# Kernel tuning notes

Measured on AMD Instinct MI355X. Metric: run time of the kernel, lower is better.

The kernel has to match this reference:

```python
import jax, jax.numpy as jnp
import numpy as np

B, C, H, W = 8, 512, 64, 64
G = 32  # GroupNorm groups
EPS = 1e-5


def setup_inputs() -> dict:
    key = jax.random.key(0)
    ks = jax.random.split(key, 5)
    x = jax.random.normal(ks[0], (B, C, H, W), dtype=jnp.float32)
    gn_w = jnp.ones((C,), jnp.float32)
    gn_b = jnp.zeros((C,), jnp.float32)
    # 1x1 convs == channel-mixing matmuls; kaiming-ish init scale
    qkv_w = jax.random.normal(ks[1], (3 * C, C), jnp.float32) / np.sqrt(C)
    qkv_b = jnp.zeros((3 * C,), jnp.float32)
    proj_w = jax.random.normal(ks[2], (C, C), jnp.float32) / np.sqrt(C)
    proj_b = jnp.zeros((C,), jnp.float32)
    return {"x": x, "gn_w": gn_w, "gn_b": gn_b, "qkv_w": qkv_w,
            "qkv_b": qkv_b, "proj_w": proj_w, "proj_b": proj_b}


def _group_norm(x, w, b):
    Bv, Cv, Hv, Wv = x.shape
    xr = x.reshape(Bv, G, Cv // G, Hv * Wv)
    mu = xr.mean(axis=(2, 3), keepdims=True)
    var = xr.var(axis=(2, 3), keepdims=True)
    xn = ((xr - mu) * jax.lax.rsqrt(var + EPS)).reshape(Bv, Cv, Hv, Wv)
    return xn * w[None, :, None, None] + b[None, :, None, None]


def reference(x, gn_w, gn_b, qkv_w, qkv_b, proj_w, proj_b):
    Bv, Cv, Hv, Wv = x.shape
    T = Hv * Wv
    h = _group_norm(x, gn_w, gn_b)
    # 1x1 conv -> [B, 3C, T]
    qkv = jnp.einsum('bchw,oc->bohw', h, qkv_w) + qkv_b[None, :, None, None]
    qkv = qkv.reshape(Bv, 3, Cv, T)
    q, k, v = qkv[:, 0], qkv[:, 1], qkv[:, 2]  # each [B, C, T]
    scale = Cv ** -0.25  # 1/sqrt(sqrt(C)), applied to q and k
    attn = jnp.einsum('bct,bcs->bts', q * scale, k * scale)  # [B, T, T]
    attn = jax.nn.softmax(attn, axis=-1)
    out = jnp.einsum('bts,bcs->bct', attn, v).reshape(Bv, Cv, Hv, Wv)
    out = jnp.einsum('bchw,oc->bohw', out, proj_w) + proj_b[None, :, None, None]
    return x + out
```

## Files before the change

### kernel.cpp

```cpp
#include <hip/hip_runtime.h>

typedef unsigned short u16;
typedef unsigned int   u32;
typedef unsigned long long u64;

typedef __attribute__((ext_vector_type(8)))  short short8;
typedef __attribute__((ext_vector_type(4)))  short short4v;
typedef __attribute__((ext_vector_type(4)))  float float4v;
typedef __attribute__((ext_vector_type(16))) float float16v;

#define NB 8
#define NC 512
#define NT 4096
#define NO 1536
#define SCALE_QK 0.04419417382415922f
#define LOG2E_   1.4426950408889634f

__device__ inline u16 f2b(float f){
  u32 u = __builtin_bit_cast(u32, f);
  u += 0x7fffu + ((u >> 16) & 1u);
  return (u16)(u >> 16);
}

typedef __attribute__((address_space(1))) const unsigned int as1c_uint;
typedef __attribute__((address_space(3))) unsigned int as3_uint;

__device__ inline void gload16(const void* g, void* l){
  __builtin_amdgcn_global_load_lds((as1c_uint*)g, (as3_uint*)l, 16, 0, 0);
}

__device__ inline short8 ld8pair(const u16* p){
  short4v a = *(const short4v*)(p);
  short4v b = *(const short4v*)(p + 4);
  return __builtin_shufflevector(a, b, 0,1,2,3,4,5,6,7);
}

__global__ void k_cvt(const float* __restrict__ src, u16* __restrict__ dst, int n){
  int i = blockIdx.x*256 + threadIdx.x;
  if (i < n) dst[i] = f2b(src[i]);
}

__global__ void k_stats(const float* __restrict__ x, float* __restrict__ stats){
  int bg = blockIdx.x;
  int tid = threadIdx.x;
  const float4* p = (const float4*)(x + (size_t)bg*65536);
  float s = 0.f, q = 0.f;
  for (int i=0;i<64;i++){
    float4 v = p[i*256 + tid];
    s += v.x+v.y+v.z+v.w;
    q += v.x*v.x + v.y*v.y + v.z*v.z + v.w*v.w;
  }
  __shared__ float ls[256], lq[256];
  ls[tid]=s; lq[tid]=q; __syncthreads();
  for (int off=128; off>0; off>>=1){
    if (tid < off){ ls[tid]+=ls[tid+off]; lq[tid]+=lq[tid+off]; }
    __syncthreads();
  }
  if (tid==0){
    float mean = ls[0]*(1.f/65536.f);
    float var  = lq[0]*(1.f/65536.f) - mean*mean;
    stats[bg*2]   = mean;
    stats[bg*2+1] = rsqrtf(var + 1e-5f);
  }
}

__global__ void k_gn_apply(const float* __restrict__ x, const float* __restrict__ stats,
                           const float* __restrict__ gw, const float* __restrict__ gb,
                           u16* __restrict__ h){
  __shared__ u16 lt[64*65];
  int b = blockIdx.z, c0 = blockIdx.y*64, t0 = blockIdx.x*64;
  int tid = threadIdx.x;
  for (int it=0; it<16; it++){
    int idx = it*256 + tid;
    int cl = idx>>6, tl = idx&63;
    int c = c0 + cl;
    float v = x[((size_t)b*NC + c)*NT + t0 + tl];
    float mean = stats[(b*32 + (c>>4))*2];
    float rstd = stats[(b*32 + (c>>4))*2 + 1];
    float y = (v - mean)*rstd*gw[c] + gb[c];
    lt[cl*65 + tl] = f2b(y);
  }
  __syncthreads();
  for (int it=0; it<16; it++){
    int idx = it*256 + tid;
    int tw = idx>>6, cw = idx&63;
    h[((size_t)b*NT + t0 + tw)*NC + c0 + cw] = lt[cw*65 + tw];
  }
}

__device__ inline void stage128(const u16* gbase, u16* lbuf, int w, int l){
  #pragma unroll
  for (int i=0;i<4;i++){
    int r0 = (w*4+i)*8;
    int lr = r0 + (l>>3);
    int gch = (l&7) ^ (lr&7);
    gload16(gbase + (size_t)lr*512 + gch*8, lbuf + r0*64);
  }
}

__device__ inline void tile_mac(const u16* sA, const u16* sB, float4v acc[4][4], int wm, int wn, int l){
  #pragma unroll
  for (int kk=0; kk<2; kk++){
    short8 af[4], bf[4];
    #pragma unroll
    for (int f=0; f<4; f++){
      int rowA = wm + f*16 + (l&15);
      int chA  = (kk*4 + (l>>4)) ^ (rowA&7);
      af[f] = *(const short8*)(sA + rowA*64 + chA*8);
      int rowB = wn + f*16 + (l&15);
      int chB  = (kk*4 + (l>>4)) ^ (rowB&7);
      bf[f] = *(const short8*)(sB + rowB*64 + chB*8);
    }
    #pragma unroll
    for (int fm=0; fm<4; fm++)
      #pragma unroll
      for (int fn=0; fn<4; fn++)
        acc[fm][fn] = __builtin_amdgcn_mfma_f32_16x16x32_bf16(af[fm], bf[fn], acc[fm][fn], 0,0,0);
  }
}

__global__ __launch_bounds__(256,2) void k_qkv_gemm(const u16* __restrict__ h, const u16* __restrict__ wq,
                                                    const float* __restrict__ qb, u16* __restrict__ qkv){
  __shared__ __align__(16) u16 lA[2][8192];
  __shared__ __align__(16) u16 lB[2][8192];
  int b = blockIdx.z, t0 = blockIdx.y*128, o0 = blockIdx.x*128;
  int tid = threadIdx.x, w = tid>>6, l = tid&63;
  int wm = (w&1)*64, wn = (w>>1)*64;
  float4v acc[4][4];
  #pragma unroll
  for (int i=0;i<4;i++)
    #pragma unroll
    for (int j=0;j<4;j++)
      #pragma unroll
      for (int e=0;e<4;e++) acc[i][j][e] = 0.f;
  const u16* Ab = h  + ((size_t)b*NT + t0)*NC;
  const u16* Bb = wq + (size_t)o0*NC;
  stage128(Ab, lA[0], w, l);
  stage128(Bb, lB[0], w, l);
  __syncthreads();
  for (int it=0; it<8; it++){
    int cur = it&1;
    if (it < 7){
      stage128(Ab + (it+1)*64, lA[cur^1], w, l);
      stage128(Bb + (it+1)*64, lB[cur^1], w, l);
    }
    tile_mac(lA[cur], lB[cur], acc, wm, wn, l);
    __syncthreads();
  }
  u16* ep = ((w < 2) ? (u16*)lA : (u16*)lB) + (w&1)*4352;
  #pragma unroll
  for (int fn=0; fn<4; fn++){
    float bs = qb[o0 + wn + fn*16 + (l&15)];
    #pragma unroll
    for (int fm=0; fm<4; fm++)
      #pragma unroll
      for (int r=0; r<4; r++){
        int tl_ = fm*16 + (l>>4)*4 + r;
        int ol_ = fn*16 + (l&15);
        ep[tl_*68 + ol_] = f2b(acc[fm][fn][r] + bs);
      }
  }
  __syncthreads();
  #pragma unroll
  for (int i=0;i<8;i++){
    int r  = i*8 + (l>>3);
    int c8 = (l&7)*8;
    short8 v8 = ld8pair(ep + r*68 + c8);
    *(short8*)(qkv + ((size_t)b*NT + t0 + wm + r)*NO + o0 + wn + c8) = v8;
  }
}

__global__ void k_vtrans(const u16* __restrict__ qkv, u16* __restrict__ vct){
  __shared__ u16 lt[64*65];
  int b = blockIdx.z, c0 = blockIdx.y*64, t0 = blockIdx.x*64;
  int tid = threadIdx.x;
  for (int it=0; it<16; it++){
    int idx = it*256 + tid;
    int tl = idx>>6, cl = idx&63;
    lt[tl*65 + cl] = qkv[((size_t)b*NT + t0+tl)*NO + 1024 + c0 + cl];
  }
  __syncthreads();
  for (int it=0; it<16; it++){
    int idx = it*256 + tid;
    int cw = idx>>6, tw = idx&63;
    vct[((size_t)b*NC + c0+cw)*NT + t0 + tw] = lt[tw*65 + cw];
  }
}

__global__ __launch_bounds__(256,2) void k_attn(const u16* __restrict__ qkv, const u16* __restrict__ vct,
                                                u16* __restrict__ at){
  __shared__ __align__(16) u16 lK[32*512];
  __shared__ __align__(16) u16 lV[512*36];
  __shared__ __align__(16) u16 lP[64*36];
  __shared__ __align__(16) float lAl[64];
  __shared__ __align__(16) float lLs[64];
  const int b = blockIdx.y, t0 = blockIdx.x*64;
  const int tid = threadIdx.x, w = tid>>6, l = tid&63;
  const int l15 = l&15, l4 = l>>4, l31 = l&31, l5 = l>>5;
  const int mq = w, pm = w>>1, pc = w&1;

  short8 qf[16];
  {
    const u16* qrow = qkv + ((size_t)b*NT + t0 + mq*16 + l15)*NO;
    #pragma unroll
    for (int ks=0; ks<16; ks++) qf[ks] = *(const short8*)(qrow + ks*32 + l4*8);
  }
  float16v acc[8];
  #pragma unroll
  for (int i=0;i<8;i++)
    #pragma unroll
    for (int j=0;j<16;j++) acc[i][j] = 0.f;
  float M_r[4] = {-1e30f,-1e30f,-1e30f,-1e30f};
  float L_r[4] = {0.f,0.f,0.f,0.f};

  for (int st=0; st<128; st++){
    const int s0 = st*32;
    #pragma unroll
    for (int i=0;i<8;i++){
      int sl = w*8 + i;
      const u16* krow = qkv + ((size_t)b*NT + s0 + sl)*NO + 512;
      gload16(krow + (l ^ (sl&7))*8, &lK[sl*512]);
    }
    #pragma unroll
    for (int rr=0; rr<2; rr++){
      int c = rr*256 + tid;
      const u64* vr = (const u64*)(vct + ((size_t)b*NC + c)*NT + s0);
      u64* dst = (u64*)(&lV[c*36]);
      #pragma unroll
      for (int i=0;i<8;i++) dst[i] = vr[i];
    }
    __syncthreads();

    float4v Lf0, Lf1;
    #pragma unroll
    for (int e=0;e<4;e++){ Lf0[e]=0.f; Lf1[e]=0.f; }
    #pragma unroll
    for (int ks=0; ks<16; ks++){
      int gch = ks*4 + l4;
      int sA = l15;
      short8 b0 = *(const short8*)(&lK[sA*512 + ((gch ^ (sA&7))*8)]);
      int sB = 16 + l15;
      short8 b1 = *(const short8*)(&lK[sB*512 + ((gch ^ (sB&7))*8)]);
      Lf0 = __builtin_amdgcn_mfma_f32_16x16x32_bf16(qf[ks], b0, Lf0, 0,0,0);
      Lf1 = __builtin_amdgcn_mfma_f32_16x16x32_bf16(qf[ks], b1, Lf1, 0,0,0);
    }
    #pragma unroll
    for (int r=0; r<4; r++){
      float v0 = Lf0[r]*SCALE_QK, v1 = Lf1[r]*SCALE_QK;
      float mx = fmaxf(v0, v1);
      mx = fmaxf(mx, __shfl_xor(mx,1));
      mx = fmaxf(mx, __shfl_xor(mx,2));
      mx = fmaxf(mx, __shfl_xor(mx,4));
      mx = fmaxf(mx, __shfl_xor(mx,8));
      float mnew = fmaxf(M_r[r], mx);
      float al = exp2f((M_r[r] - mnew)*LOG2E_);
      float p0 = exp2f((v0 - mnew)*LOG2E_);
      float p1 = exp2f((v1 - mnew)*LOG2E_);
      float sum = p0 + p1;
      sum += __shfl_xor(sum,1); sum += __shfl_xor(sum,2);
      sum += __shfl_xor(sum,4); sum += __shfl_xor(sum,8);
      L_r[r] = L_r[r]*al + sum;
      M_r[r] = mnew;
      int tl_ = mq*16 + l4*4 + r;
      lP[tl_*36 + l15]      = f2b(p0);
      lP[tl_*36 + 16 + l15] = f2b(p1);
      if (l15 == 0) lAl[tl_] = al;
    }
    __syncthreads();

    {
      float4v a_[4];
      #pragma unroll
      for (int q=0;q<4;q++) a_[q] = *(const float4v*)(&lAl[pm*32 + q*8 + l5*4]);
      #pragma unroll
      for (int fn=0; fn<8; fn++)
        #pragma unroll
        for (int q=0;q<4;q++)
          #pragma unroll
          for (int rr=0;rr<4;rr++) acc[fn][q*4+rr] *= a_[q][rr];

      const u16* prow = &lP[(pm*32 + l31)*36];
      short8 pa0 = ld8pair(prow + l5*8);
      short8 pa1 = ld8pair(prow + 16 + l5*8);
      #pragma unroll
      for (int fn=0; fn<8; fn++){
        const u16* vrow = &lV[(pc*256 + fn*32 + l31)*36];
        short8 vb0 = ld8pair(vrow + l5*8);
        short8 vb1 = ld8pair(vrow + 16 + l5*8);
        acc[fn] = __builtin_amdgcn_mfma_f32_32x32x16_bf16(pa0, vb0, acc[fn], 0,0,0);
        acc[fn] = __builtin_amdgcn_mfma_f32_32x32x16_bf16(pa1, vb1, acc[fn], 0,0,0);
      }
    }
    __syncthreads();
  }

  if (l15 == 0){
    #pragma unroll
    for (int r=0;r<4;r++) lLs[mq*16 + l4*4 + r] = L_r[r];
  }
  __syncthreads();
  {
    float4v iv[4];
    #pragma unroll
    for (int q=0;q<4;q++){
      float4v t_ = *(const float4v*)(&lLs[pm*32 + q*8 + l5*4]);
      #pragma unroll
      for (int rr=0;rr<4;rr++) iv[q][rr] = 1.f/t_[rr];
    }
    #pragma unroll
    for (int fn=0; fn<8; fn++){
      int cc = pc*256 + fn*32 + l31;
      #pragma unroll
      for (int q=0;q<4;q++)
        #pragma unroll
        for (int rr=0;rr<4;rr++){
          int tt = t0 + pm*32 + rr + q*8 + l5*4;
          at[((size_t)b*NT + tt)*NC + cc] = f2b(acc[fn][q*4+rr]*iv[q][rr]);
        }
    }
  }
}

__global__ __launch_bounds__(256,2) void k_proj_res(const u16* __restrict__ wp, const u16* __restrict__ at,
                                                    const float* __restrict__ pb, const float* __restrict__ x,
                                                    float* __restrict__ out){
  __shared__ __align__(16) u16 lA[2][8192];
  __shared__ __align__(16) u16 lB[2][8192];
  int b = blockIdx.z, t0 = blockIdx.x*128, o0 = blockIdx.y*128;
  int tid = threadIdx.x, w = tid>>6, l = tid&63;
  int wm = (w&1)*64, wn = (w>>1)*64;
  float4v acc[4][4];
  #pragma unroll
  for (int i=0;i<4;i++)
    #pragma unroll
    for (int j=0;j<4;j++)
      #pragma unroll
      for (int e=0;e<4;e++) acc[i][j][e] = 0.f;
  const u16* Ab = wp + (size_t)o0*NC;
  const u16* Bb = at + ((size_t)b*NT + t0)*NC;
  stage128(Ab, lA[0], w, l);
  stage128(Bb, lB[0], w, l);
  __syncthreads();
  for (int it=0; it<8; it++){
    int cur = it&1;
    if (it < 7){
      stage128(Ab + (it+1)*64, lA[cur^1], w, l);
      stage128(Bb + (it+1)*64, lB[cur^1], w, l);
    }
    tile_mac(lA[cur], lB[cur], acc, wm, wn, l);
    __syncthreads();
  }
  #pragma unroll
  for (int fm=0; fm<4; fm++)
    #pragma unroll
    for (int r=0; r<4; r++){
      int o = o0 + wm + fm*16 + (l>>4)*4 + r;
      float bs = pb[o];
      #pragma unroll
      for (int fn=0; fn<4; fn++){
        int t = t0 + wn + fn*16 + (l&15);
        size_t idx = ((size_t)b*NC + o)*NT + t;
        out[idx] = acc[fm][fn][r] + bs + x[idx];
      }
    }
}

extern "C" void kernel_launch(void* const* d_in, const int* in_sizes, int n_in,
                              void* d_out, int out_size, void* d_ws, size_t ws_size,
                              hipStream_t stream){
  const float* x    = (const float*)d_in[0];
  const float* gnw  = (const float*)d_in[1];
  const float* gnb  = (const float*)d_in[2];
  const float* qkvw = (const float*)d_in[3];
  const float* qkvb = (const float*)d_in[4];
  const float* pw   = (const float*)d_in[5];
  const float* pb   = (const float*)d_in[6];
  float* out = (float*)d_out;

  char* ws = (char*)d_ws;
  float* stats = (float*)ws;
  u16* h   = (u16*)(ws + 4096);
  u16* qkv = (u16*)(ws + 4096 + 33554432);
  u16* vct = (u16*)(ws + 4096 + 33554432 + 100663296);
  u16* wqb = (u16*)(ws + 4096 + 33554432 + 100663296 + 33554432);
  u16* wpb = (u16*)(ws + 4096 + 33554432 + 100663296 + 33554432 + 1572864);
  u16* at  = h;

  k_cvt<<<3072, 256, 0, stream>>>(qkvw, wqb, 786432);
  k_cvt<<<1024, 256, 0, stream>>>(pw, wpb, 262144);
  k_stats<<<256, 256, 0, stream>>>(x, stats);
  k_gn_apply<<<dim3(64,8,8), 256, 0, stream>>>(x, stats, gnw, gnb, h);
  k_qkv_gemm<<<dim3(12,32,8), 256, 0, stream>>>(h, wqb, qkvb, qkv);
  k_vtrans<<<dim3(64,8,8), 256, 0, stream>>>(qkv, vct);
  k_attn<<<dim3(64,8), 256, 0, stream>>>(qkv, vct, at);
  k_proj_res<<<dim3(32,4,8), 256, 0, stream>>>(wpb, at, pb, x, out);
}
```

Before: 1.118 ms.

## Double-buffer K/V tiles in attention with 512-thread blocks of 128 queries

The attention kernel now processes 128 queries per block using 512 threads. It double-buffers the K and V tiles in shared memory: the next K tile is fetched asynchronously and the next V tile is staged in registers while the current tile is computed. This is meant to hide global-load latency behind the MFMA work and to halve K/V refetches across blocks. The grid is flattened with batch in the low bits. In exchange it doubles LDS use and drops to one block per CU, and it adds an explicit barrier plus setprio around the PV MFMAs.

```diff
diff --git a/kernel.cpp b/kernel.cpp
--- a/kernel.cpp
+++ b/kernel.cpp
@@ -187,21 +187,23 @@
   }
 }
 
-__global__ __launch_bounds__(256,2) void k_attn(const u16* __restrict__ qkv, const u16* __restrict__ vct,
+__global__ __launch_bounds__(512,1) void k_attn(const u16* __restrict__ qkv, const u16* __restrict__ vct,
                                                 u16* __restrict__ at){
-  __shared__ __align__(16) u16 lK[32*512];
-  __shared__ __align__(16) u16 lV[512*36];
-  __shared__ __align__(16) u16 lP[64*36];
-  __shared__ __align__(16) float lAl[64];
-  __shared__ __align__(16) float lLs[64];
-  const int b = blockIdx.y, t0 = blockIdx.x*64;
+  __shared__ __align__(16) u16 lK[2][32*512];
+  __shared__ __align__(16) u16 lV[2][512*36];
+  __shared__ __align__(16) u16 lP[128*36];
+  __shared__ __align__(16) float lAl[128];
+  __shared__ __align__(16) float lLs[128];
+  const int bid = blockIdx.x;
+  const int b = bid & 7;
+  const int t0 = (bid >> 3) * 128;
   const int tid = threadIdx.x, w = tid>>6, l = tid&63;
   const int l15 = l&15, l4 = l>>4, l31 = l&31, l5 = l>>5;
-  const int mq = w, pm = w>>1, pc = w&1;
+  const int pm = w>>1, pc = w&1;
 
   short8 qf[16];
   {
-    const u16* qrow = qkv + ((size_t)b*NT + t0 + mq*16 + l15)*NO;
+    const u16* qrow = qkv + ((size_t)b*NT + t0 + w*16 + l15)*NO;
     #pragma unroll
     for (int ks=0; ks<16; ks++) qf[ks] = *(const short8*)(qrow + ks*32 + l4*8);
   }
@@ -213,23 +215,37 @@
   float M_r[4] = {-1e30f,-1e30f,-1e30f,-1e30f};
   float L_r[4] = {0.f,0.f,0.f,0.f};
 
+  u64 vreg[8];
+  const u64* vrow = (const u64*)(vct + ((size_t)b*NC + tid)*NT);
+
+  #pragma unroll
+  for (int i=0;i<4;i++){
+    int sl = w*4+i;
+    const u16* krow = qkv + ((size_t)b*NT + sl)*NO + 512;
+    gload16(krow + (l ^ (sl&7))*8, &lK[0][sl*512]);
+  }
+  #pragma unroll
+  for (int i=0;i<8;i++) vreg[i] = vrow[i];
+  {
+    u64* dst = (u64*)(&lV[0][tid*36]);
+    #pragma unroll
+    for (int i=0;i<8;i++) dst[i] = vreg[i];
+  }
+  __syncthreads();
+
+  int cur = 0;
   for (int st=0; st<128; st++){
-    const int s0 = st*32;
-    #pragma unroll
-    for (int i=0;i<8;i++){
-      int sl = w*8 + i;
-      const u16* krow = qkv + ((size_t)b*NT + s0 + sl)*NO + 512;
-      gload16(krow + (l ^ (sl&7))*8, &lK[sl*512]);
-    }
-    #pragma unroll
-    for (int rr=0; rr<2; rr++){
-      int c = rr*256 + tid;
-      const u64* vr = (const u64*)(vct + ((size_t)b*NC + c)*NT + s0);
-      u64* dst = (u64*)(&lV[c*36]);
-      #pragma unroll
-      for (int i=0;i<8;i++) dst[i] = vr[i];
-    }
-    __syncthreads();
+    if (st < 127){
+      const int s1 = st*32 + 32;
+      #pragma unroll
+      for (int i=0;i<4;i++){
+        int sl = w*4+i;
+        const u16* krow = qkv + ((size_t)b*NT + s1 + sl)*NO + 512;
+        gload16(krow + (l ^ (sl&7))*8, &lK[cur^1][sl*512]);
+      }
+      #pragma unroll
+      for (int i=0;i<8;i++) vreg[i] = vrow[(size_t)(st+1)*8 + i];
+    }
 
     float4v Lf0, Lf1;
     #pragma unroll
@@ -238,12 +254,13 @@
     for (int ks=0; ks<16; ks++){
       int gch = ks*4 + l4;
       int sA = l15;
-      short8 b0 = *(const short8*)(&lK[sA*512 + ((gch ^ (sA&7))*8)]);
+      short8 b0 = *(const short8*)(&lK[cur][sA*512 + ((gch ^ (sA&7))*8)]);
       int sB = 16 + l15;
-      short8 b1 = *(const short8*)(&lK[sB*512 + ((gch ^ (sB&7))*8)]);
+      short8 b1 = *(const short8*)(&lK[cur][sB*512 + ((gch ^ (sB&7))*8)]);
       Lf0 = __builtin_amdgcn_mfma_f32_16x16x32_bf16(qf[ks], b0, Lf0, 0,0,0);
       Lf1 = __builtin_amdgcn_mfma_f32_16x16x32_bf16(qf[ks], b1, Lf1, 0,0,0);
     }
+
     #pragma unroll
     for (int r=0; r<4; r++){
       float v0 = Lf0[r]*SCALE_QK, v1 = Lf1[r]*SCALE_QK;
@@ -261,12 +278,16 @@
       sum += __shfl_xor(sum,4); sum += __shfl_xor(sum,8);
       L_r[r] = L_r[r]*al + sum;
       M_r[r] = mnew;
-      int tl_ = mq*16 + l4*4 + r;
+      int tl_ = w*16 + l4*4 + r;
       lP[tl_*36 + l15]      = f2b(p0);
       lP[tl_*36 + 16 + l15] = f2b(p1);
       if (l15 == 0) lAl[tl_] = al;
     }
-    __syncthreads();
+
+    asm volatile("s_waitcnt lgkmcnt(0)" ::: "memory");
+    __builtin_amdgcn_sched_barrier(0);
+    __builtin_amdgcn_s_barrier();
+    __builtin_amdgcn_sched_barrier(0);
 
     {
       float4v a_[4];
@@ -282,21 +303,30 @@
       const u16* prow = &lP[(pm*32 + l31)*36];
       short8 pa0 = ld8pair(prow + l5*8);
       short8 pa1 = ld8pair(prow + 16 + l5*8);
+      __builtin_amdgcn_s_setprio(1);
       #pragma unroll
       for (int fn=0; fn<8; fn++){
-        const u16* vrow = &lV[(pc*256 + fn*32 + l31)*36];
-        short8 vb0 = ld8pair(vrow + l5*8);
-        short8 vb1 = ld8pair(vrow + 16 + l5*8);
+        const u16* vr_ = &lV[cur][(pc*256 + fn*32 + l31)*36];
+        short8 vb0 = ld8pair(vr_ + l5*8);
+        short8 vb1 = ld8pair(vr_ + 16 + l5*8);
         acc[fn] = __builtin_amdgcn_mfma_f32_32x32x16_bf16(pa0, vb0, acc[fn], 0,0,0);
         acc[fn] = __builtin_amdgcn_mfma_f32_32x32x16_bf16(pa1, vb1, acc[fn], 0,0,0);
       }
+      __builtin_amdgcn_s_setprio(0);
+    }
+
+    if (st < 127){
+      u64* dst = (u64*)(&lV[cur^1][tid*36]);
+      #pragma unroll
+      for (int i=0;i<8;i++) dst[i] = vreg[i];
     }
     __syncthreads();
+    cur ^= 1;
   }
 
   if (l15 == 0){
     #pragma unroll
-    for (int r=0;r<4;r++) lLs[mq*16 + l4*4 + r] = L_r[r];
+    for (int r=0;r<4;r++) lLs[w*16 + l4*4 + r] = L_r[r];
   }
   __syncthreads();
   {
@@ -392,6 +422,6 @@
   k_gn_apply<<<dim3(64,8,8), 256, 0, stream>>>(x, stats, gnw, gnb, h);
   k_qkv_gemm<<<dim3(12,32,8), 256, 0, stream>>>(h, wqb, qkvb, qkv);
   k_vtrans<<<dim3(64,8,8), 256, 0, stream>>>(qkv, vct);
-  k_attn<<<dim3(64,8), 256, 0, stream>>>(qkv, vct, at);
+  k_attn<<<256, 512, 0, stream>>>(qkv, vct, at);
   k_proj_res<<<dim3(32,4,8), 256, 0, stream>>>(wpb, at, pb, x, out);
 }
```

Result: slower. 1.410 ms (+26.1%).
